# Kernel tuning notes

Measured on AMD Instinct MI355X. Metric: run time of the kernel, lower is better.

## Reference

```python
import jax, jax.numpy as jnp
import numpy as np

N, IN_DIM, H, ATT_DIM, OUT_DIM = 4096, 512, 8, 64, 64
ATT_BIAS = 0.5


def setup_inputs() -> dict:
    key = jax.random.key(0)
    ks = jax.random.split(key, 12)
    s_in = 1.0 / np.sqrt(IN_DIM)
    s_o = 1.0 / np.sqrt(H * OUT_DIM)
    return {
        "Q": jax.random.normal(ks[0], (N, IN_DIM), jnp.float32),
        "K": jax.random.normal(ks[1], (N, IN_DIM), jnp.float32),
        "V": jax.random.normal(ks[2], (N, IN_DIM), jnp.float32),
        "adj": jax.random.uniform(ks[3], (N, N), jnp.float32),
        "WQ": jax.random.normal(ks[4], (IN_DIM, H * ATT_DIM), jnp.float32) * s_in,
        "bQ": jnp.zeros((H * ATT_DIM,), jnp.float32),
        "WK": jax.random.normal(ks[5], (IN_DIM, H * ATT_DIM), jnp.float32) * s_in,
        "bK": jnp.zeros((H * ATT_DIM,), jnp.float32),
        "WV": jax.random.normal(ks[6], (IN_DIM, H * OUT_DIM), jnp.float32) * s_in,
        "bV": jnp.zeros((H * OUT_DIM,), jnp.float32),
        "WO": jax.random.normal(ks[7], (H * OUT_DIM, OUT_DIM), jnp.float32) * s_o,
        "bO": jnp.zeros((OUT_DIM,), jnp.float32),
    }


def reference(Q, K, V, adj, WQ, bQ, WK, bK, WV, bV, WO, bO):
    scale = ATT_DIM ** -0.5
    q = (Q @ WQ + bQ).reshape(N, H, ATT_DIM)   # [N,H,d]
    k = (K @ WK + bK).reshape(N, H, ATT_DIM)   # [N,H,d]
    v = (V @ WV + bV).reshape(N, H, OUT_DIM)   # [N,H,e]
    # scaled QK^T per head: [H,N,N]
    scores = jnp.einsum("nhd,mhd->hnm", q * scale, k)
    # sigmoid -> bias subtract -> +0.1*adj -> softmax over keys
    scores = jax.nn.sigmoid(scores) - ATT_BIAS + 0.1 * adj[None, :, :]
    attn = jax.nn.softmax(scores, axis=2)
    # attend values (dropout p=0 => identity), concat heads, project
    out = jnp.einsum("hnm,mhe->nhe", attn, v).reshape(N, H * OUT_DIM)
    return out @ WO + bO
```

## Files before the change

kernel.cpp:

```cpp
#include <hip/hip_runtime.h>
#include <hip/hip_bf16.h>

#define N_TOK  4096
#define HD     512
#define NH     8
#define NSPLIT 4
#define QBLK   128
#define NT     ((N_TOK / NSPLIT) / 64)

typedef short v8s __attribute__((ext_vector_type(8)));
typedef float v4f __attribute__((ext_vector_type(4)));
typedef float v16f __attribute__((ext_vector_type(16)));
typedef unsigned short u16;

#define QSCALE   0.18033688011112042f
#define ADJ2     0.14426950408889634f
#define EA0 0.999410f
#define EA1 1.016220f
#define EA2 0.423120f
#define EA3 0.279120f

__device__ __forceinline__ float bf2f(u16 x) {
  union { unsigned int u; float f; } c; c.u = ((unsigned int)x) << 16; return c.f;
}
__device__ __forceinline__ u16 f2bf(float f) {
  union { float f; unsigned int u; } c; c.f = f;
  return (u16)((c.u + 0x7fffu + ((c.u >> 16) & 1u)) >> 16);
}
__device__ __forceinline__ float fast_exp2(float x) {
#if __has_builtin(__builtin_amdgcn_exp2f)
  return __builtin_amdgcn_exp2f(x);
#else
  return exp2f(x);
#endif
}
__device__ __forceinline__ unsigned int pk_bf16(float a, float b) {
  union { __hip_bfloat162 h; unsigned int u; } c;
  c.h = __float22bfloat162_rn(make_float2(a, b));
  return c.u;
}

typedef __attribute__((address_space(1))) const char gchar;
typedef __attribute__((address_space(3))) char lchar;
__device__ __forceinline__ void glds16(const void* g, void* l) {
  __builtin_amdgcn_global_load_lds((gchar*)g, (lchar*)l, 16, 0, 0);
}
__device__ __forceinline__ void plswap(unsigned int& a, unsigned int& b) {
  asm volatile("v_permlane32_swap_b32 %0, %1" : "+v"(a), "+v"(b));
}

__device__ __forceinline__ bool detect_f32(const u16* __restrict__ q) {
  int l = threadIdx.x & 63;
  u16 e = q[2 * l];
  float x = bf2f(e);
  int ex = (e >> 7) & 0xFF;
  float ax = fabsf(x);
  bool ok = (ex != 0xFF) && (ax < 64.f) && (ax > 1e-30f);
  unsigned long long m = __ballot(ok);
  return __popcll(m) < 48;
}
__device__ __forceinline__ float bias_ld(const void* b, int i, bool f32) {
  return f32 ? ((const float*)b)[i] : bf2f(((const u16*)b)[i]);
}

__global__ __launch_bounds__(256) void conv_adjE_k(const void* __restrict__ adj, u16* __restrict__ adjE,
                                                   const u16* __restrict__ Qdet) {
  bool f32 = detect_f32(Qdet);
  int i = blockIdx.x * 256 + threadIdx.x;
  float4 f;
  if (f32) {
    f = ((const float4*)adj)[i];
  } else {
    short4 v = ((const short4*)adj)[i];
    f.x = bf2f((u16)v.x); f.y = bf2f((u16)v.y); f.z = bf2f((u16)v.z); f.w = bf2f((u16)v.w);
  }
  unsigned int d0 = pk_bf16(fast_exp2(f.x * ADJ2), fast_exp2(f.y * ADJ2));
  unsigned int d1 = pk_bf16(fast_exp2(f.z * ADJ2), fast_exp2(f.w * ADJ2));
  ((uint2*)adjE)[i] = make_uint2(d0, d1);
}

__global__ __launch_bounds__(256) void conv_qkv_k(const void* __restrict__ A0, const void* __restrict__ A1,
                                                  const void* __restrict__ A2,
                                                  u16* __restrict__ c0, u16* __restrict__ c1,
                                                  u16* __restrict__ c2, const u16* __restrict__ Qdet) {
  bool f32 = detect_f32(Qdet);
  int z = blockIdx.y;
  const void* in = (z == 0) ? A0 : (z == 1) ? A1 : A2;
  u16* out       = (z == 0) ? c0 : (z == 1) ? c1 : c2;
  int i = blockIdx.x * 256 + threadIdx.x;
  if (f32) {
    const float* sp = (const float*)in + (size_t)i * 8;
    float4 a = *(const float4*)sp, b = *(const float4*)(sp + 4);
    uint4 q = make_uint4(pk_bf16(a.x, a.y), pk_bf16(a.z, a.w),
                         pk_bf16(b.x, b.y), pk_bf16(b.z, b.w));
    *(uint4*)(out + (size_t)i * 8) = q;
  } else {
    *(v8s*)(out + (size_t)i * 8) = *(const v8s*)((const u16*)in + (size_t)i * 8);
  }
}

__global__ __launch_bounds__(256) void tr_w_k(const void* W0, const void* W1, const void* W2, const void* W3,
                                              u16* t0, u16* t1, u16* t2, u16* t3,
                                              const u16* __restrict__ Qdet) {
  bool f32 = detect_f32(Qdet);
  int z = blockIdx.z;
  const void* in; u16* out; int C;
  if (z == 0)      { in = W0; out = t0; C = 512; }
  else if (z == 1) { in = W1; out = t1; C = 512; }
  else if (z == 2) { in = W2; out = t2; C = 512; }
  else             { in = W3; out = t3; C = 64; if (blockIdx.y) return; }
  const int R = 512;
  __shared__ __align__(16) u16 tile[64][72];
  const int r0 = blockIdx.x * 64, c0 = blockIdx.y * 64;
  const int t = threadIdx.x;
#pragma unroll
  for (int rep = 0; rep < 2; ++rep) {
    int idx = (t + rep * 256) * 8;
    int r = idx >> 6, c = idx & 63;
    if (f32) {
      const float* sp = (const float*)in + (size_t)(r0 + r) * C + (c0 + c);
      float4 a = *(const float4*)sp, b = *(const float4*)(sp + 4);
      uint4 q = make_uint4(pk_bf16(a.x, a.y), pk_bf16(a.z, a.w),
                           pk_bf16(b.x, b.y), pk_bf16(b.z, b.w));
      *(uint4*)&tile[r][c] = q;
    } else {
      *(v8s*)&tile[r][c] = *(const v8s*)((const u16*)in + (size_t)(r0 + r) * C + (c0 + c));
    }
  }
  __syncthreads();
#pragma unroll
  for (int rep = 0; rep < 2; ++rep) {
    int idx = (t + rep * 256) * 8;
    int oc = idx >> 6, orr = idx & 63;
    u16 tmp[8];
#pragma unroll
    for (int j = 0; j < 8; ++j) tmp[j] = tile[orr + j][oc];
    *(v8s*)(out + (size_t)(c0 + oc) * R + (r0 + orr)) = *(v8s*)tmp;
  }
}

__global__ __launch_bounds__(256) void gemm_qkv_k(const u16* __restrict__ c0, const u16* __restrict__ c1,
                                                  const u16* __restrict__ c2,
                                                  const u16* __restrict__ t0, const u16* __restrict__ t1,
                                                  const u16* __restrict__ t2,
                                                  const void* b0, const void* b1, const void* b2,
                                                  u16* __restrict__ qb, u16* __restrict__ kb,
                                                  u16* __restrict__ vtb, const u16* __restrict__ Qdet) {
  __shared__ __align__(16) u16 As[64][72];
  __shared__ __align__(16) u16 Bs[64][72];
  bool f32 = detect_f32(Qdet);
  int z = blockIdx.z;
  const u16* Abf = (z == 0) ? c0 : (z == 1) ? c1 : c2;
  const u16* Bt  = (z == 0) ? t0 : (z == 1) ? t1 : t2;
  const void* bias = (z == 0) ? b0 : (z == 1) ? b1 : b2;
  const bool vt = (z == 2);
  const int i0 = blockIdx.x * 64, j0 = blockIdx.y * 64;
  const int t = threadIdx.x, w = t >> 6, l = t & 63, quad = l >> 4, l15 = l & 15;
  v4f acc[4] = {};
  for (int k0 = 0; k0 < 512; k0 += 64) {
#pragma unroll
    for (int rep = 0; rep < 2; ++rep) {
      int idx = (t + rep * 256) * 8;
      int r = idx >> 6, c = idx & 63;
      *(v8s*)&As[r][c] = *(const v8s*)(Abf + (size_t)(i0 + r) * 512 + k0 + c);
      *(v8s*)&Bs[r][c] = *(const v8s*)(Bt + (size_t)(j0 + r) * 512 + k0 + c);
    }
    __syncthreads();
    if (vt) {
#pragma unroll
      for (int h = 0; h < 2; ++h) {
        v8s a = *(const v8s*)&As[w * 16 + l15][h * 32 + quad * 8];
#pragma unroll
        for (int cb = 0; cb < 4; ++cb) {
          v8s b = *(const v8s*)&Bs[cb * 16 + l15][h * 32 + quad * 8];
          acc[cb] = __builtin_amdgcn_mfma_f32_16x16x32_bf16(b, a, acc[cb], 0, 0, 0);
        }
      }
    } else {
#pragma unroll
      for (int h = 0; h < 2; ++h) {
        v8s a = *(const v8s*)&As[w * 16 + l15][h * 32 + quad * 8];
#pragma unroll
        for (int cb = 0; cb < 4; ++cb) {
          v8s b = *(const v8s*)&Bs[cb * 16 + l15][h * 32 + quad * 8];
          acc[cb] = __builtin_amdgcn_mfma_f32_16x16x32_bf16(a, b, acc[cb], 0, 0, 0);
        }
      }
    }
    __syncthreads();
  }
  if (vt) {
#pragma unroll
    for (int cb = 0; cb < 4; ++cb) {
#pragma unroll
      for (int r = 0; r < 4; ++r) {
        int jj = j0 + cb * 16 + quad * 4 + r;
        int ii = i0 + w * 16 + l15;
        vtb[(size_t)jj * N_TOK + ii] = f2bf(acc[cb][r] + bias_ld(bias, jj, f32));
      }
    }
  } else {
    const float oscale = (z == 0) ? QSCALE : 1.0f;
    u16* C = (z == 0) ? qb : kb;
#pragma unroll
    for (int cb = 0; cb < 4; ++cb) {
      int col = j0 + cb * 16 + l15;
      float bv = bias_ld(bias, col, f32);
#pragma unroll
      for (int r = 0; r < 4; ++r) {
        int row = i0 + w * 16 + quad * 4 + r;
        C[(size_t)row * HD + col] = f2bf((acc[cb][r] + bv) * oscale);
      }
    }
  }
}

__global__ __launch_bounds__(256, 4) void attn_kernel(const u16* __restrict__ qb, const u16* __restrict__ kb,
                                                      const u16* __restrict__ vtb, const u16* __restrict__ adjE,
                                                      u16* __restrict__ Opart, float* __restrict__ Lpart) {
  __shared__ __align__(16) u16 Ks[2][64 * 64];
  __shared__ __align__(16) u16 Vs[2][64 * 64];
  const int i0 = blockIdx.x * QBLK, h64 = blockIdx.y * 64, z = blockIdx.z;
  const int t = threadIdx.x, w = t >> 6, l = t & 63;
  const int il = l & 31, h2 = l >> 5, il7 = il & 7;
  const int iRow = i0 + w * 32 + il;

  v8s qf[4];
#pragma unroll
  for (int c = 0; c < 4; ++c)
    qf[c] = *(const v8s*)(qb + (size_t)iRow * HD + h64 + 16 * c + 8 * h2);

  const u16* adjRow = adjE + (size_t)iRow * N_TOK + 4 * h2;

  const int srow = l >> 3;
  const int scol = ((l & 7) ^ srow) * 8;
  const int ldsrow = 16 * w;

  v16f oacc0 = {}, oacc1 = {};
  float lsum = 0.f;
  const int m_begin = z * (N_TOK / NSPLIT);

#pragma unroll
  for (int n = 0; n < 2; ++n) {
    int r = ldsrow + 8 * n + srow;
    glds16(kb + (size_t)(m_begin + r) * HD + h64 + scol, &Ks[0][(ldsrow + 8 * n) * 64]);
    glds16(vtb + (size_t)(h64 + r) * N_TOK + m_begin + scol, &Vs[0][(ldsrow + 8 * n) * 64]);
  }
  __syncthreads();

  int buf = 0;
  for (int mt = 0; mt < NT; ++mt) {
    const int m0 = m_begin + mt * 64;
    if (mt + 1 < NT) {
      const int m1 = m0 + 64;
#pragma unroll
      for (int n = 0; n < 2; ++n) {
        int r = ldsrow + 8 * n + srow;
        glds16(kb + (size_t)(m1 + r) * HD + h64 + scol, &Ks[buf ^ 1][(ldsrow + 8 * n) * 64]);
        glds16(vtb + (size_t)(h64 + r) * N_TOK + m1 + scol, &Vs[buf ^ 1][(ldsrow + 8 * n) * 64]);
      }
    }
    const u16* Kb = &Ks[buf][0];
    const u16* Vb = &Vs[buf][0];

#pragma unroll
    for (int mh = 0; mh < 2; ++mh) {
      uint2 av[4];
#pragma unroll
      for (int rq = 0; rq < 4; ++rq)
        av[rq] = *(const uint2*)(adjRow + m0 + 32 * mh + 8 * rq);

      v16f macc = {};
      __builtin_amdgcn_s_setprio(1);
#pragma unroll
      for (int c = 0; c < 4; ++c) {
        v8s kf = *(const v8s*)(Kb + (32 * mh + il) * 64 + (((2 * c + h2) ^ il7) * 8));
        macc = __builtin_amdgcn_mfma_f32_32x32x16_bf16(kf, qf[c], macc, 0, 0, 0);
      }
      __builtin_amdgcn_s_setprio(0);

      float p[16];
#pragma unroll
      for (int rq = 0; rq < 4; ++rq) {
        union { unsigned int u; float f; } e0, e1, e2, e3;
        e0.u = av[rq].x << 16; e1.u = av[rq].x & 0xFFFF0000u;
        e2.u = av[rq].y << 16; e3.u = av[rq].y & 0xFFFF0000u;
        float r0 = __builtin_amdgcn_rcpf(1.f + fast_exp2(-macc[4 * rq + 0]));
        float r1 = __builtin_amdgcn_rcpf(1.f + fast_exp2(-macc[4 * rq + 1]));
        float r2 = __builtin_amdgcn_rcpf(1.f + fast_exp2(-macc[4 * rq + 2]));
        float r3 = __builtin_amdgcn_rcpf(1.f + fast_exp2(-macc[4 * rq + 3]));
        float p0 = e0.f * fmaf(fmaf(fmaf(EA3, r0, EA2), r0, EA1), r0, EA0);
        float p1 = e1.f * fmaf(fmaf(fmaf(EA3, r1, EA2), r1, EA1), r1, EA0);
        float p2 = e2.f * fmaf(fmaf(fmaf(EA3, r2, EA2), r2, EA1), r2, EA0);
        float p3 = e3.f * fmaf(fmaf(fmaf(EA3, r3, EA2), r3, EA1), r3, EA0);
        lsum += (p0 + p1) + (p2 + p3);
        p[4 * rq + 0] = p0; p[4 * rq + 1] = p1; p[4 * rq + 2] = p2; p[4 * rq + 3] = p3;
      }

      v8s pf[2];
#pragma unroll
      for (int sub = 0; sub < 2; ++sub) {
        unsigned int u0 = pk_bf16(p[8 * sub + 0], p[8 * sub + 1]);
        unsigned int u1 = pk_bf16(p[8 * sub + 2], p[8 * sub + 3]);
        unsigned int u2 = pk_bf16(p[8 * sub + 4], p[8 * sub + 5]);
        unsigned int u3 = pk_bf16(p[8 * sub + 6], p[8 * sub + 7]);
        plswap(u0, u2); plswap(u1, u3);
        union { uint4 q; v8s v; } pu;
        pu.q = make_uint4(u0, u1, u2, u3);
        pf[sub] = pu.v;
      }

      __builtin_amdgcn_s_setprio(1);
#pragma unroll
      for (int sub = 0; sub < 2; ++sub) {
        const int mc = 2 * mh + sub;
        v8s vf0 = *(const v8s*)(Vb + (il) * 64      + (((2 * mc + h2) ^ il7) * 8));
        v8s vf1 = *(const v8s*)(Vb + (32 + il) * 64 + (((2 * mc + h2) ^ il7) * 8));
        oacc0 = __builtin_amdgcn_mfma_f32_32x32x16_bf16(pf[sub], vf0, oacc0, 0, 0, 0);
        oacc1 = __builtin_amdgcn_mfma_f32_32x32x16_bf16(pf[sub], vf1, oacc1, 0, 0, 0);
      }
      __builtin_amdgcn_s_setprio(0);
    }
    __syncthreads();
    buf ^= 1;
  }

  lsum += __shfl_xor(lsum, 32);
  if (l < 32)
    Lpart[((size_t)z * N_TOK + i0 + 32 * w + il) * NH + blockIdx.y] = lsum;

#pragma unroll
  for (int r = 0; r < 16; ++r) {
    int i_local = (r & 3) + 8 * (r >> 2) + 4 * h2;
    size_t row = (size_t)z * N_TOK + i0 + 32 * w + i_local;
    u16* op = Opart + row * HD + h64 + il;
    op[0]  = f2bf(oacc0[r]);
    op[32] = f2bf(oacc1[r]);
  }
}

__global__ __launch_bounds__(256) void gemm_bt(const u16* __restrict__ Opart, const float* __restrict__ Lpart,
                                               const u16* __restrict__ Bt, const void* bias,
                                               void* __restrict__ C, const u16* __restrict__ Qdet) {
  __shared__ __align__(16) u16 As[16][72];
  __shared__ __align__(16) u16 Bs[64][72];
  bool f32 = detect_f32(Qdet);
  const int i0 = blockIdx.x * 16;
  const int t = threadIdx.x, w = t >> 6, l = t & 63, quad = l >> 4, l15 = l & 15;
  v4f acc = {};
  for (int k0 = 0; k0 < 512; k0 += 64) {
    const int h = k0 >> 6;
    if (t < 128) {
      int row = t >> 3, c8 = (t & 7) * 8;
      float lv = 0.f;
#pragma unroll
      for (int s = 0; s < NSPLIT; ++s) lv += Lpart[((size_t)s * N_TOK + i0 + row) * NH + h];
      float rl = __builtin_amdgcn_rcpf(lv);
      float vals[8] = {};
#pragma unroll
      for (int s = 0; s < NSPLIT; ++s) {
        v8s ov = *(const v8s*)(Opart + ((size_t)s * N_TOK + i0 + row) * HD + k0 + c8);
#pragma unroll
        for (int j = 0; j < 8; ++j) vals[j] += bf2f((u16)ov[j]);
      }
      uint4 q = make_uint4(pk_bf16(vals[0] * rl, vals[1] * rl), pk_bf16(vals[2] * rl, vals[3] * rl),
                           pk_bf16(vals[4] * rl, vals[5] * rl), pk_bf16(vals[6] * rl, vals[7] * rl));
      *(uint4*)&As[row][c8] = q;
    }
#pragma unroll
    for (int rep = 0; rep < 2; ++rep) {
      int idx = (t + rep * 256) * 8;
      int r = idx >> 6, c = idx & 63;
      *(v8s*)&Bs[r][c] = *(const v8s*)(Bt + (size_t)r * 512 + k0 + c);
    }
    __syncthreads();
#pragma unroll
    for (int h2 = 0; h2 < 2; ++h2) {
      v8s a = *(const v8s*)&As[l15][h2 * 32 + quad * 8];
      v8s b = *(const v8s*)&Bs[w * 16 + l15][h2 * 32 + quad * 8];
      acc = __builtin_amdgcn_mfma_f32_16x16x32_bf16(a, b, acc, 0, 0, 0);
    }
    __syncthreads();
  }
  {
    int col = w * 16 + l15;
    float bv = bias_ld(bias, col, f32);
#pragma unroll
    for (int r = 0; r < 4; ++r) {
      int row = i0 + quad * 4 + r;
      float v = acc[r] + bv;
      size_t idx = (size_t)row * 64 + col;
      if (f32) ((float*)C)[idx] = v;
      else     ((u16*)C)[idx] = f2bf(v);
    }
  }
}

extern "C" void kernel_launch(void* const* d_in, const int* in_sizes, int n_in,
                              void* d_out, int out_size, void* d_ws, size_t ws_size,
                              hipStream_t stream) {
  (void)in_sizes; (void)n_in; (void)out_size; (void)ws_size;
  const void* Q   = d_in[0];
  const void* K   = d_in[1];
  const void* V   = d_in[2];
  const void* adj = d_in[3];
  const void* WQ  = d_in[4];
  const void* bQ  = d_in[5];
  const void* WK  = d_in[6];
  const void* bK  = d_in[7];
  const void* WV  = d_in[8];
  const void* bV  = d_in[9];
  const void* WO  = d_in[10];
  const void* bO  = d_in[11];
  const u16* Qdet = (const u16*)Q;

  char* p = (char*)d_ws;
  auto alloc = [&](size_t bytes) { char* r = p; p += (bytes + 255) & ~(size_t)255; return r; };
  const size_t SZ = (size_t)N_TOK * HD * 2;

  u16* adjE    = (u16*)alloc((size_t)N_TOK * N_TOK * 2);
  u16* qb      = (u16*)alloc(SZ);
  u16* kb      = (u16*)alloc(SZ);
  u16* vtb     = (u16*)alloc(SZ);
  u16* Opart   = (u16*)alloc((size_t)NSPLIT * SZ);
  float* Lpart = (float*)alloc((size_t)NSPLIT * N_TOK * NH * 4);
  u16* tQ      = (u16*)alloc((size_t)512 * 512 * 2);
  u16* tK      = (u16*)alloc((size_t)512 * 512 * 2);
  u16* tV      = (u16*)alloc((size_t)512 * 512 * 2);
  u16* tO      = (u16*)alloc((size_t)64 * 512 * 2);
  u16* Qc      = (u16*)alloc(SZ);
  u16* Kc      = (u16*)alloc(SZ);
  u16* Vc      = (u16*)alloc(SZ);

  dim3 b256(256);
  conv_adjE_k<<<dim3(16384), b256, 0, stream>>>(adj, adjE, Qdet);
  conv_qkv_k<<<dim3(1024, 3), b256, 0, stream>>>(Q, K, V, Qc, Kc, Vc, Qdet);
  tr_w_k<<<dim3(8, 8, 4), b256, 0, stream>>>(WQ, WK, WV, WO, tQ, tK, tV, tO, Qdet);
  gemm_qkv_k<<<dim3(64, 8, 3), b256, 0, stream>>>(Qc, Kc, Vc, tQ, tK, tV,
                                                  bQ, bK, bV, qb, kb, vtb, Qdet);
  attn_kernel<<<dim3(N_TOK / QBLK, NH, NSPLIT), b256, 0, stream>>>(qb, kb, vtb, adjE, Opart, Lpart);
  gemm_bt<<<dim3(256), b256, 0, stream>>>(Opart, Lpart, tO, bO, d_out, Qdet);
}
```

Before: 253.6 us.

## Double-buffer QKV projection GEMM with direct global-to-LDS loads and XOR swizzle

```diff
diff --git a/kernel.cpp b/kernel.cpp
--- a/kernel.cpp
+++ b/kernel.cpp
@@ -146,8 +146,8 @@
                                                   const void* b0, const void* b1, const void* b2,
                                                   u16* __restrict__ qb, u16* __restrict__ kb,
                                                   u16* __restrict__ vtb, const u16* __restrict__ Qdet) {
-  __shared__ __align__(16) u16 As[64][72];
-  __shared__ __align__(16) u16 Bs[64][72];
+  __shared__ __align__(16) u16 As[2][64 * 64];
+  __shared__ __align__(16) u16 Bs[2][64 * 64];
   bool f32 = detect_f32(Qdet);
   int z = blockIdx.z;
   const u16* Abf = (z == 0) ? c0 : (z == 1) ? c1 : c2;
@@ -156,39 +156,53 @@
   const bool vt = (z == 2);
   const int i0 = blockIdx.x * 64, j0 = blockIdx.y * 64;
   const int t = threadIdx.x, w = t >> 6, l = t & 63, quad = l >> 4, l15 = l & 15;
+  const int srow = l >> 3;
+  const int scol = ((l & 7) ^ srow) * 8;
+  const int ldsrow = 16 * w;
+
+#define STG(BUF, K0)                                                         \
+  _Pragma("unroll") for (int n_ = 0; n_ < 2; ++n_) {                         \
+    int r_ = ldsrow + 8 * n_ + srow;                                         \
+    glds16(Abf + (size_t)(i0 + r_) * 512 + (K0) + scol,                      \
+           (u16*)As[BUF] + (ldsrow + 8 * n_) * 64);                          \
+    glds16(Bt + (size_t)(j0 + r_) * 512 + (K0) + scol,                       \
+           (u16*)Bs[BUF] + (ldsrow + 8 * n_) * 64);                          \
+  }
+
   v4f acc[4] = {};
-  for (int k0 = 0; k0 < 512; k0 += 64) {
-#pragma unroll
-    for (int rep = 0; rep < 2; ++rep) {
-      int idx = (t + rep * 256) * 8;
-      int r = idx >> 6, c = idx & 63;
-      *(v8s*)&As[r][c] = *(const v8s*)(Abf + (size_t)(i0 + r) * 512 + k0 + c);
-      *(v8s*)&Bs[r][c] = *(const v8s*)(Bt + (size_t)(j0 + r) * 512 + k0 + c);
-    }
-    __syncthreads();
-    if (vt) {
-#pragma unroll
-      for (int h = 0; h < 2; ++h) {
-        v8s a = *(const v8s*)&As[w * 16 + l15][h * 32 + quad * 8];
+  STG(0, 0)
+  __syncthreads();
+  int buf = 0;
+  for (int kt = 0; kt < 8; ++kt) {
+    if (kt + 1 < 8) {
+      STG(buf ^ 1, (kt + 1) * 64)
+    }
+    const u16* Ab = As[buf];
+    const u16* Bb = Bs[buf];
+    const int arow = w * 16 + l15;
+#pragma unroll
+    for (int h = 0; h < 2; ++h) {
+      v8s a = *(const v8s*)(Ab + arow * 64 + (((h * 4 + quad) ^ (arow & 7)) * 8));
+      if (vt) {
 #pragma unroll
         for (int cb = 0; cb < 4; ++cb) {
-          v8s b = *(const v8s*)&Bs[cb * 16 + l15][h * 32 + quad * 8];
+          const int brow = cb * 16 + l15;
+          v8s b = *(const v8s*)(Bb + brow * 64 + (((h * 4 + quad) ^ (brow & 7)) * 8));
           acc[cb] = __builtin_amdgcn_mfma_f32_16x16x32_bf16(b, a, acc[cb], 0, 0, 0);
         }
-      }
-    } else {
-#pragma unroll
-      for (int h = 0; h < 2; ++h) {
-        v8s a = *(const v8s*)&As[w * 16 + l15][h * 32 + quad * 8];
+      } else {
 #pragma unroll
         for (int cb = 0; cb < 4; ++cb) {
-          v8s b = *(const v8s*)&Bs[cb * 16 + l15][h * 32 + quad * 8];
+          const int brow = cb * 16 + l15;
+          v8s b = *(const v8s*)(Bb + brow * 64 + (((h * 4 + quad) ^ (brow & 7)) * 8));
           acc[cb] = __builtin_amdgcn_mfma_f32_16x16x32_bf16(a, b, acc[cb], 0, 0, 0);
         }
       }
     }
     __syncthreads();
-  }
+    buf ^= 1;
+  }
+#undef STG
   if (vt) {
 #pragma unroll
     for (int cb = 0; cb < 4; ++cb) {
```

Result: no change. 249.3 us (-1.7%).
